# Kernel tuning notes

Measured on AMD Instinct MI355X. Metric: run time of the kernel, lower is better.

## Reference

```python
import jax, jax.numpy as jnp
import numpy as np

B, S, D_IN, D_OUT = 4, 2048, 1024, 1024


def setup_inputs() -> dict:
    key = jax.random.key(0)
    kx, kq, kk, kv = jax.random.split(key, 4)
    scale = 1.0 / np.sqrt(D_IN)
    return {
        "x": jax.random.normal(kx, (B, S, D_IN), dtype=jnp.float32),
        "W_q": jax.random.normal(kq, (D_IN, D_OUT), dtype=jnp.float32) * scale,
        "W_k": jax.random.normal(kk, (D_IN, D_OUT), dtype=jnp.float32) * scale,
        "W_v": jax.random.normal(kv, (D_IN, D_OUT), dtype=jnp.float32) * scale,
    }


def reference(x, W_q, W_k, W_v):
    # QKV projections (Linear without bias): [B,S,D_out]
    q = jnp.einsum("bsd,de->bse", x, W_q)
    k = jnp.einsum("bsd,de->bse", x, W_k)
    v = jnp.einsum("bsd,de->bse", x, W_v)

    # Raw scores [B,S,S], causal mask (strict upper triangle -> -inf),
    # then scale by sqrt(d_k) and softmax, matching the torch order of ops.
    scores = jnp.einsum("bqd,bkd->bqk", q, k)
    seq = scores.shape[-1]
    causal = jnp.triu(jnp.ones((seq, seq), dtype=bool), k=1)
    scores = jnp.where(causal[None, :, :], -jnp.inf, scores)
    attn = jax.nn.softmax(scores / jnp.sqrt(jnp.asarray(q.shape[-1], scores.dtype)), axis=-1)
    # dropout p=0.0 -> identity (eval semantics)
    return jnp.einsum("bqk,bkd->bqd", attn, v)
```

## Files before the change

### kernel.cpp

```cpp
#include <hip/hip_runtime.h>

typedef unsigned short u16;
typedef __bf16 bf16x8 __attribute__((ext_vector_type(8)));
typedef float f32x4 __attribute__((ext_vector_type(4)));

__device__ __forceinline__ u16 f2bf(float f) {
    union { float f; unsigned int u; } v; v.f = f;
    unsigned int u = v.u;
    return (u16)((u + 0x7FFFu + ((u >> 16) & 1u)) >> 16);
}

__device__ __forceinline__ void load_lds16(const void* g, void* l) {
    __builtin_amdgcn_global_load_lds(
        (const __attribute__((address_space(1))) unsigned int*)g,
        (__attribute__((address_space(3))) unsigned int*)l,
        16, 0, 0);
}

__constant__ unsigned char cls_m[24] = {15,15,7,14,14,13,13,6,12,12,11,11,5,10,10,9,9,4,8,8,3,2,1,0};
__constant__ unsigned char cls_h[24] = { 0, 1,2, 0, 1, 0, 1,2, 0, 1, 0, 1,2, 0, 1,0,1,2,0,1,2,2,2,2};

__global__ void __launch_bounds__(256) prep_kernel(
    const float4* __restrict__ X, u16* __restrict__ xb,
    const float* __restrict__ Wq, const float* __restrict__ Wk,
    const float* __restrict__ Wv,
    u16* __restrict__ Oq, u16* __restrict__ Ok, u16* __restrict__ Ov,
    float* __restrict__ rowsum) {
    __shared__ float tile[32][33];
    const int bid = blockIdx.x, tid = threadIdx.x;
    if (bid < 8192) {
        int idx = bid * 256 + tid;
        float4 v = X[idx];
        ushort4 o;
        o.x = f2bf(v.x); o.y = f2bf(v.y); o.z = f2bf(v.z); o.w = f2bf(v.w);
        *(ushort4*)(xb + (size_t)idx * 4) = o;
    } else if (bid < 11264) {
        int id = bid - 8192;
        int zz = id >> 10;
        const float* W = (zz == 0) ? Wq : (zz == 1) ? Wk : Wv;
        u16* O = (zz == 0) ? Oq : (zz == 1) ? Ok : Ov;
        int n0 = (id & 31) * 32, k0 = ((id >> 5) & 31) * 32;
        int tx = tid & 31, ty = tid >> 5;
        #pragma unroll
        for (int j = 0; j < 32; j += 8)
            tile[ty + j][tx] = W[(size_t)(k0 + ty + j) * 1024 + n0 + tx];
        __syncthreads();
        #pragma unroll
        for (int j = 0; j < 32; j += 8)
            O[(size_t)(n0 + ty + j) * 1024 + k0 + tx] = f2bf(tile[tx][ty + j]);
    } else {
        rowsum[(bid - 11264) * 256 + tid] = 0.f;
    }
}

__global__ void __launch_bounds__(256) combine_kernel(
    const float4* __restrict__ P1, const float* __restrict__ rowsum,
    float4* __restrict__ out) {
    int b = blockIdx.x;
    int z = b >> 10;
    int i = (b & 1023) * 256 + threadIdx.x;
    int r = i >> 8;
    float inv = 1.0f / rowsum[z * 2048 + 1024 + r];
    size_t oi = (size_t)z * (2048 * 1024 / 4) + (1024 * 1024 / 4) + i;
    float4 a = out[oi];
    float4 p = P1[(size_t)z * (1024 * 1024 / 4) + i];
    a.x = (a.x + p.x) * inv;
    a.y = (a.y + p.y) * inv;
    a.z = (a.z + p.z) * inv;
    a.w = (a.w + p.w) * inv;
    out[oi] = a;
}

template <int MODE>
__global__ void __launch_bounds__(512) gemm_nt(
    const u16* __restrict__ xb, const u16* __restrict__ WqT,
    const u16* __restrict__ WkT, const u16* __restrict__ WvT,
    u16* __restrict__ Q, u16* __restrict__ Kb,
    u16* __restrict__ Vt, u16* __restrict__ S,
    float* __restrict__ rowsum, float* __restrict__ out,
    float* __restrict__ P1) {

    int mtile, ntile, z, kbeg = 0, kiters, kh = 2;
    const u16 *A, *B;

    if (MODE == 0) {
        int L = blockIdx.x;
        int c = L & 7, t = (L >> 3) & 7, hi = L >> 6;
        int p = hi * 8 + c;
        z = p >> 6; mtile = p & 63; ntile = t;
        A = xb;
        B = (z == 0) ? WqT : (z == 1) ? WkT : WvT;
        kiters = 16;
    } else if (MODE == 1) {
        int id2 = blockIdx.x;
        z = id2 / 192;
        int r = id2 - z * 192;
        int c = r & 7, g = r >> 3;
        if (g <= c)            { mtile = c;     ntile = g; }
        else if (g < 2*c + 10) { mtile = c + 8; ntile = g - (c + 1); }
        else return;
        A = Q  + (size_t)z * (2048 * 1024);
        B = Kb + (size_t)z * (2048 * 1024);
        kiters = 16;
    } else {
        int L = blockIdx.x;
        ntile = L & 7;
        int j = L >> 3;
        z = j & 3;
        int ci = j >> 2;
        mtile = cls_m[ci];
        kh = cls_h[ci];
        kbeg = (kh != 2) ? kh * (mtile + 1) : 0;
        kiters = (kh != 2) ? (mtile + 1) : (mtile + 1) * 2;
        A = S  + (size_t)z * (2048 * 2048);
        B = Vt + (size_t)z * (1024 * 2048);
    }

    const int LDA = (MODE == 2) ? 2048 : 1024;

    __shared__ __align__(16) u16 As[128 * 64];
    __shared__ __align__(16) u16 Bs[128 * 64 + MODE * 256];

    const int tid = threadIdx.x;
    const int lane = tid & 63;
    const int wave = tid >> 6;
    const int wr = wave >> 2, wc = wave & 3;

    const int r0 = tid >> 2;
    const int kb = (((tid & 3) ^ ((r0 >> 1) & 3))) * 16;

    const char* gA = (const char*)(A + (size_t)(mtile * 128 + r0) * LDA) + kb + kbeg * 128;
    const char* gB = (const char*)(B + (size_t)(ntile * 128 + r0) * LDA) + kb + kbeg * 128;

    char* lA = (char*)As + tid * 16;
    char* lB = (char*)Bs + tid * 16;

    f32x4 acc[4][2] = {};

    const int quad = lane >> 4;
    const int l16 = lane & 15;
    const int ch = quad ^ ((l16 >> 1) & 3);
    const int aoff = (wr * 64 + l16) * 32 + ch * 8;
    const int boff = (wc * 32 + l16) * 32 + ch * 8;

    for (int kt = 0; kt < kiters; ++kt) {
        load_lds16(gA,      lA);
        load_lds16(gA + 64, lA + 8192);
        load_lds16(gB,      lB);
        load_lds16(gB + 64, lB + 8192);
        gA += 128; gB += 128;
        __syncthreads();

        #pragma unroll
        for (int h = 0; h < 2; ++h) {
            const u16* ap = As + h * 4096 + aoff;
            const u16* bp = Bs + h * 4096 + boff;
            bf16x8 af[4], bfv[2];
            #pragma unroll
            for (int r = 0; r < 4; ++r) af[r] = *(const bf16x8*)(ap + r * 512);
            #pragma unroll
            for (int c = 0; c < 2; ++c) bfv[c] = *(const bf16x8*)(bp + c * 512);
            #pragma unroll
            for (int r = 0; r < 4; ++r)
                #pragma unroll
                for (int c = 0; c < 2; ++c)
                    acc[r][c] = __builtin_amdgcn_mfma_f32_16x16x32_bf16(
                        af[r], bfv[c], acc[r][c], 0, 0, 0);
        }
        __syncthreads();
    }

    const int grow0 = mtile * 128 + wr * 64 + quad * 4;
    const int gcol0 = ntile * 128 + wc * 32 + l16;

    if (MODE == 0) {
        if (z < 2) {
            u16* C = z ? Kb : Q;
            #pragma unroll
            for (int r = 0; r < 4; ++r)
                #pragma unroll
                for (int c = 0; c < 2; ++c)
                    #pragma unroll
                    for (int i = 0; i < 4; ++i)
                        C[(size_t)(grow0 + r * 16 + i) * 1024 + gcol0 + c * 16] =
                            f2bf(acc[r][c][i]);
        } else {
            #pragma unroll
            for (int r = 0; r < 4; ++r) {
                int m0 = grow0 + r * 16;
                int b = m0 >> 11, s0 = m0 & 2047;
                #pragma unroll
                for (int c = 0; c < 2; ++c) {
                    int d = gcol0 + c * 16;
                    ushort4 o;
                    o.x = f2bf(acc[r][c][0]); o.y = f2bf(acc[r][c][1]);
                    o.z = f2bf(acc[r][c][2]); o.w = f2bf(acc[r][c][3]);
                    *(ushort4*)(Vt + (size_t)b * (1024 * 2048) + (size_t)d * 2048 + s0) = o;
                }
            }
        }
    } else if (MODE == 1) {
        u16* C = S + (size_t)z * (2048 * 2048);
        float* rs = rowsum + z * 2048;
        const bool diag = (ntile == mtile);
        float rsum[4][4];
        #pragma unroll
        for (int r = 0; r < 4; ++r)
            #pragma unroll
            for (int i = 0; i < 4; ++i) rsum[r][i] = 0.f;
        #pragma unroll
        for (int r = 0; r < 4; ++r)
            #pragma unroll
            for (int c = 0; c < 2; ++c)
                #pragma unroll
                for (int i = 0; i < 4; ++i) {
                    int grow = grow0 + r * 16 + i;
                    int gcol = gcol0 + c * 16;
                    float e = 0.f;
                    if (!diag || gcol <= grow)
                        e = __expf(acc[r][c][i] * 0.03125f - 12.0f);
                    C[(size_t)grow * 2048 + gcol] = f2bf(e);
                    rsum[r][i] += e;
                }
        #pragma unroll
        for (int r = 0; r < 4; ++r)
            #pragma unroll
            for (int i = 0; i < 4; ++i) {
                float s = rsum[r][i];
                s += __shfl_xor(s, 1, 64);
                s += __shfl_xor(s, 2, 64);
                s += __shfl_xor(s, 4, 64);
                s += __shfl_xor(s, 8, 64);
                if (l16 == 0)
                    unsafeAtomicAdd(&rs[grow0 + r * 16 + i], s);
            }
    } else {
        if (kh == 2) {
            const float* rs = rowsum + z * 2048;
            float* C = out + (size_t)z * (2048 * 1024);
            #pragma unroll
            for (int r = 0; r < 4; ++r)
                #pragma unroll
                for (int i = 0; i < 4; ++i) {
                    int grow = grow0 + r * 16 + i;
                    float inv = 1.0f / rs[grow];
                    #pragma unroll
                    for (int c = 0; c < 2; ++c)
                        C[(size_t)grow * 1024 + gcol0 + c * 16] = acc[r][c][i] * inv;
                }
        } else if (kh == 1) {
            float* C = out + (size_t)z * (2048 * 1024);
            #pragma unroll
            for (int r = 0; r < 4; ++r)
                #pragma unroll
                for (int i = 0; i < 4; ++i) {
                    int grow = grow0 + r * 16 + i;
                    #pragma unroll
                    for (int c = 0; c < 2; ++c)
                        C[(size_t)grow * 1024 + gcol0 + c * 16] = acc[r][c][i];
                }
        } else {
            float* Pp = P1 + (size_t)z * (1024 * 1024);
            #pragma unroll
            for (int r = 0; r < 4; ++r)
                #pragma unroll
                for (int i = 0; i < 4; ++i) {
                    int prow = grow0 + r * 16 + i - 1024;
                    #pragma unroll
                    for (int c = 0; c < 2; ++c)
                        Pp[(size_t)prow * 1024 + gcol0 + c * 16] = acc[r][c][i];
                }
        }
    }
}

extern "C" void kernel_launch(void* const* d_in, const int* in_sizes, int n_in,
                              void* d_out, int out_size, void* d_ws, size_t ws_size,
                              hipStream_t stream) {
    const float* x  = (const float*)d_in[0];
    const float* Wq = (const float*)d_in[1];
    const float* Wk = (const float*)d_in[2];
    const float* Wv = (const float*)d_in[3];
    float* out = (float*)d_out;
    char* ws = (char*)d_ws;
    const size_t Mi = 1u << 20;

    u16* xb  = (u16*)(ws);
    u16* WqT = (u16*)(ws + 16 * Mi);
    u16* WkT = (u16*)(ws + 18 * Mi);
    u16* WvT = (u16*)(ws + 20 * Mi);
    u16* Q   = (u16*)(ws + 22 * Mi);
    u16* Kb  = (u16*)(ws + 38 * Mi);
    u16* Vt  = (u16*)(ws + 54 * Mi);
    u16* S   = (u16*)(ws + 70 * Mi);
    float* rowsum = (float*)(ws + 102 * Mi);
    float* P1 = (float*)xb;

    prep_kernel<<<11296, 256, 0, stream>>>(
        (const float4*)x, xb, Wq, Wk, Wv, WqT, WkT, WvT, rowsum);

    gemm_nt<0><<<1536, 512, 0, stream>>>(xb, WqT, WkT, WvT, Q, Kb, Vt, S, rowsum, out, P1);

    gemm_nt<1><<<768, 512, 0, stream>>>(xb, WqT, WkT, WvT, Q, Kb, Vt, S, rowsum, out, P1);

    gemm_nt<2><<<768, 512, 0, stream>>>(xb, WqT, WkT, WvT, Q, Kb, Vt, S, rowsum, out, P1);

    combine_kernel<<<4096, 256, 0, stream>>>(
        (const float4*)P1, rowsum, (float4*)out);
}
```

Before: 227.7 us.

## Use 256x256 double-buffered pipelined GEMM for scores and PV stages

Splits the QKV projection into its own kernel and gives the QK^T and PV GEMMs a new 256x256-tile kernel. The new kernel double-buffers operands in a 128KB LDS region, prefetches the next k-slices in sub-stages between MFMA groups, and uses explicit waitcnt, barriers and setprio for scheduling. Larger tiles raise arithmetic intensity and the pipeline hides global load latency. In exchange, launch counts drop to 256 and 192 blocks, which may underfill the GPU, and causal tiles now have coarser granularity.

```diff
diff --git a/kernel.cpp b/kernel.cpp
--- a/kernel.cpp
+++ b/kernel.cpp
@@ -17,8 +17,8 @@
         16, 0, 0);
 }
 
-__constant__ unsigned char cls_m[24] = {15,15,7,14,14,13,13,6,12,12,11,11,5,10,10,9,9,4,8,8,3,2,1,0};
-__constant__ unsigned char cls_h[24] = { 0, 1,2, 0, 1, 0, 1,2, 0, 1, 0, 1,2, 0, 1,0,1,2,0,1,2,2,2,2};
+__constant__ unsigned char c2m[12] = {7,7,3,6,6,5,5,2,4,4,1,0};
+__constant__ unsigned char c2h[12] = {0,1,2,0,1,0,1,2,0,1,2,2};
 
 __global__ void __launch_bounds__(256) prep_kernel(
     const float4* __restrict__ X, u16* __restrict__ xb,
@@ -71,55 +71,20 @@
     out[oi] = a;
 }
 
-template <int MODE>
-__global__ void __launch_bounds__(512) gemm_nt(
+__global__ void __launch_bounds__(512) gemm_qkv(
     const u16* __restrict__ xb, const u16* __restrict__ WqT,
     const u16* __restrict__ WkT, const u16* __restrict__ WvT,
-    u16* __restrict__ Q, u16* __restrict__ Kb,
-    u16* __restrict__ Vt, u16* __restrict__ S,
-    float* __restrict__ rowsum, float* __restrict__ out,
-    float* __restrict__ P1) {
-
-    int mtile, ntile, z, kbeg = 0, kiters, kh = 2;
-    const u16 *A, *B;
-
-    if (MODE == 0) {
-        int L = blockIdx.x;
-        int c = L & 7, t = (L >> 3) & 7, hi = L >> 6;
-        int p = hi * 8 + c;
-        z = p >> 6; mtile = p & 63; ntile = t;
-        A = xb;
-        B = (z == 0) ? WqT : (z == 1) ? WkT : WvT;
-        kiters = 16;
-    } else if (MODE == 1) {
-        int id2 = blockIdx.x;
-        z = id2 / 192;
-        int r = id2 - z * 192;
-        int c = r & 7, g = r >> 3;
-        if (g <= c)            { mtile = c;     ntile = g; }
-        else if (g < 2*c + 10) { mtile = c + 8; ntile = g - (c + 1); }
-        else return;
-        A = Q  + (size_t)z * (2048 * 1024);
-        B = Kb + (size_t)z * (2048 * 1024);
-        kiters = 16;
-    } else {
-        int L = blockIdx.x;
-        ntile = L & 7;
-        int j = L >> 3;
-        z = j & 3;
-        int ci = j >> 2;
-        mtile = cls_m[ci];
-        kh = cls_h[ci];
-        kbeg = (kh != 2) ? kh * (mtile + 1) : 0;
-        kiters = (kh != 2) ? (mtile + 1) : (mtile + 1) * 2;
-        A = S  + (size_t)z * (2048 * 2048);
-        B = Vt + (size_t)z * (1024 * 2048);
-    }
-
-    const int LDA = (MODE == 2) ? 2048 : 1024;
+    u16* __restrict__ Q, u16* __restrict__ Kb, u16* __restrict__ Vt) {
+
+    int L = blockIdx.x;
+    int c = L & 7, t = (L >> 3) & 7, hi = L >> 6;
+    int p = hi * 8 + c;
+    int z = p >> 6, mtile = p & 63, ntile = t;
+    const u16* A = xb;
+    const u16* B = (z == 0) ? WqT : (z == 1) ? WkT : WvT;
 
     __shared__ __align__(16) u16 As[128 * 64];
-    __shared__ __align__(16) u16 Bs[128 * 64 + MODE * 256];
+    __shared__ __align__(16) u16 Bs[128 * 64];
 
     const int tid = threadIdx.x;
     const int lane = tid & 63;
@@ -129,8 +94,8 @@
     const int r0 = tid >> 2;
     const int kb = (((tid & 3) ^ ((r0 >> 1) & 3))) * 16;
 
-    const char* gA = (const char*)(A + (size_t)(mtile * 128 + r0) * LDA) + kb + kbeg * 128;
-    const char* gB = (const char*)(B + (size_t)(ntile * 128 + r0) * LDA) + kb + kbeg * 128;
+    const char* gA = (const char*)(A + (size_t)(mtile * 128 + r0) * 1024) + kb;
+    const char* gB = (const char*)(B + (size_t)(ntile * 128 + r0) * 1024) + kb;
 
     char* lA = (char*)As + tid * 16;
     char* lB = (char*)Bs + tid * 16;
@@ -143,7 +108,7 @@
     const int aoff = (wr * 64 + l16) * 32 + ch * 8;
     const int boff = (wc * 32 + l16) * 32 + ch * 8;
 
-    for (int kt = 0; kt < kiters; ++kt) {
+    for (int kt = 0; kt < 16; ++kt) {
         load_lds16(gA,      lA);
         load_lds16(gA + 64, lA + 8192);
         load_lds16(gB,      lB);
@@ -159,13 +124,13 @@
             #pragma unroll
             for (int r = 0; r < 4; ++r) af[r] = *(const bf16x8*)(ap + r * 512);
             #pragma unroll
-            for (int c = 0; c < 2; ++c) bfv[c] = *(const bf16x8*)(bp + c * 512);
+            for (int cc = 0; cc < 2; ++cc) bfv[cc] = *(const bf16x8*)(bp + cc * 512);
             #pragma unroll
             for (int r = 0; r < 4; ++r)
                 #pragma unroll
-                for (int c = 0; c < 2; ++c)
-                    acc[r][c] = __builtin_amdgcn_mfma_f32_16x16x32_bf16(
-                        af[r], bfv[c], acc[r][c], 0, 0, 0);
+                for (int cc = 0; cc < 2; ++cc)
+                    acc[r][cc] = __builtin_amdgcn_mfma_f32_16x16x32_bf16(
+                        af[r], bfv[cc], acc[r][cc], 0, 0, 0);
         }
         __syncthreads();
     }
@@ -173,102 +138,258 @@
     const int grow0 = mtile * 128 + wr * 64 + quad * 4;
     const int gcol0 = ntile * 128 + wc * 32 + l16;
 
-    if (MODE == 0) {
-        if (z < 2) {
-            u16* C = z ? Kb : Q;
-            #pragma unroll
-            for (int r = 0; r < 4; ++r)
-                #pragma unroll
-                for (int c = 0; c < 2; ++c)
-                    #pragma unroll
-                    for (int i = 0; i < 4; ++i)
-                        C[(size_t)(grow0 + r * 16 + i) * 1024 + gcol0 + c * 16] =
-                            f2bf(acc[r][c][i]);
-        } else {
-            #pragma unroll
-            for (int r = 0; r < 4; ++r) {
-                int m0 = grow0 + r * 16;
-                int b = m0 >> 11, s0 = m0 & 2047;
-                #pragma unroll
-                for (int c = 0; c < 2; ++c) {
-                    int d = gcol0 + c * 16;
-                    ushort4 o;
-                    o.x = f2bf(acc[r][c][0]); o.y = f2bf(acc[r][c][1]);
-                    o.z = f2bf(acc[r][c][2]); o.w = f2bf(acc[r][c][3]);
-                    *(ushort4*)(Vt + (size_t)b * (1024 * 2048) + (size_t)d * 2048 + s0) = o;
-                }
+    if (z < 2) {
+        u16* C = z ? Kb : Q;
+        #pragma unroll
+        for (int r = 0; r < 4; ++r)
+            #pragma unroll
+            for (int cc = 0; cc < 2; ++cc)
+                #pragma unroll
+                for (int i = 0; i < 4; ++i)
+                    C[(size_t)(grow0 + r * 16 + i) * 1024 + gcol0 + cc * 16] =
+                        f2bf(acc[r][cc][i]);
+    } else {
+        #pragma unroll
+        for (int r = 0; r < 4; ++r) {
+            int m0 = grow0 + r * 16;
+            int b = m0 >> 11, s0 = m0 & 2047;
+            #pragma unroll
+            for (int cc = 0; cc < 2; ++cc) {
+                int d = gcol0 + cc * 16;
+                ushort4 o;
+                o.x = f2bf(acc[r][cc][0]); o.y = f2bf(acc[r][cc][1]);
+                o.z = f2bf(acc[r][cc][2]); o.w = f2bf(acc[r][cc][3]);
+                *(ushort4*)(Vt + (size_t)b * (1024 * 2048) + (size_t)d * 2048 + s0) = o;
             }
         }
-    } else if (MODE == 1) {
+    }
+}
+
+template <int MODE>
+__global__ void __launch_bounds__(512) gemm8(
+    const u16* __restrict__ Q, const u16* __restrict__ Kb,
+    const u16* __restrict__ Vt, u16* __restrict__ S,
+    float* __restrict__ rowsum, float* __restrict__ out,
+    float* __restrict__ P1) {
+
+    int mtile, ntile, z, kbeg = 0, nt, kh = 2;
+    const u16 *A, *B;
+    int LDA;
+
+    if (MODE == 1) {
+        int L = blockIdx.x;
+        z = L >> 6;
+        int w = L & 63;
+        mtile = w >> 3; ntile = w & 7;
+        if (ntile > mtile) return;
+        A = Q  + (size_t)z * (2048 * 1024);
+        B = Kb + (size_t)z * (2048 * 1024);
+        nt = 16; LDA = 1024;
+    } else {
+        int L = blockIdx.x;
+        ntile = L & 3;
+        z = (L >> 2) & 3;
+        int ci = L >> 4;
+        mtile = c2m[ci]; kh = c2h[ci];
+        int half = 2 * (mtile + 1);
+        if (kh == 0)      { kbeg = 0;    nt = half; }
+        else if (kh == 1) { kbeg = half; nt = half; }
+        else              { kbeg = 0;    nt = 4 * (mtile + 1); }
+        A = S  + (size_t)z * (2048 * 2048);
+        B = Vt + (size_t)z * (1024 * 2048);
+        LDA = 2048;
+    }
+
+    __shared__ __align__(16) char LDSc[131072];
+
+    const int tid  = threadIdx.x;
+    const int lane = tid & 63;
+    const int wave = tid >> 6;
+    const int wr = wave >> 2;
+    const int wc = wave & 3;
+    const int quad = lane >> 4, l16 = lane & 15;
+    const int ch = quad ^ ((l16 >> 1) & 3);
+
+    const int sl = tid >> 2;
+    const int sc = ((tid & 3) ^ ((sl >> 1) & 3)) * 16;
+    const int gAr = mtile * 256 + (sl & 63) + ((sl >> 6) << 7);
+    const int gBr = ntile * 256 + (sl & 31) + ((sl >> 5) << 6);
+    const char* gp0 = (const char*)(A + (size_t)gAr * LDA) + sc + kbeg * 128;
+    const char* gp1 = (const char*)(A + (size_t)(gAr + 64) * LDA) + sc + kbeg * 128;
+    const char* gp2 = (const char*)(B + (size_t)gBr * LDA) + sc + kbeg * 128;
+    const char* gp3 = (const char*)(B + (size_t)(gBr + 32) * LDA) + sc + kbeg * 128;
+
+#define STG(kind, gp, t) do { \
+        char* lb_ = LDSc + (((t) & 1) << 16) + ((kind) << 14) + tid * 16; \
+        const char* g_ = (gp) + (size_t)(t) * 128; \
+        load_lds16(g_,      lb_); \
+        load_lds16(g_ + 64, lb_ + 8192); } while (0)
+
+    const int aBase = (wr * 64 + l16) * 64 + ch * 16;
+    const int bBase = 32768 + (wc * 32 + l16) * 64 + ch * 16;
+
+    f32x4 acc[8][4] = {};
+    bf16x8 af[4][2], b0[2][2], b1[2][2];
+
+    STG(0, gp0, 0); STG(2, gp2, 0); STG(1, gp1, 0); STG(3, gp3, 0);
+    if (nt > 1) { STG(0, gp0, 1); STG(3, gp3, 1); STG(1, gp1, 1); }
+    if (nt > 1) asm volatile("s_waitcnt vmcnt(6)" ::: "memory");
+    else        asm volatile("s_waitcnt vmcnt(0)" ::: "memory");
+    __builtin_amdgcn_s_barrier();
+    __builtin_amdgcn_sched_barrier(0);
+
+    for (int u = 0; u < nt; ++u) {
+        const int bo = (u & 1) << 16;
+        #pragma unroll
+        for (int a = 0; a < 4; ++a)
+            #pragma unroll
+            for (int k = 0; k < 2; ++k)
+                af[a][k] = *(const bf16x8*)(LDSc + bo + k * 8192 + a * 1024 + aBase);
+        #pragma unroll
+        for (int f = 0; f < 2; ++f)
+            #pragma unroll
+            for (int k = 0; k < 2; ++k)
+                b0[f][k] = *(const bf16x8*)(LDSc + bo + k * 8192 + f * 1024 + bBase);
+        if (u + 1 < nt) STG(2, gp2, u + 1);
+        __builtin_amdgcn_s_barrier();
+        __builtin_amdgcn_s_setprio(1);
+        #pragma unroll
+        for (int k = 0; k < 2; ++k)
+            #pragma unroll
+            for (int a = 0; a < 4; ++a)
+                #pragma unroll
+                for (int f = 0; f < 2; ++f)
+                    acc[a][f] = __builtin_amdgcn_mfma_f32_16x16x32_bf16(
+                        af[a][k], b0[f][k], acc[a][f], 0, 0, 0);
+        __builtin_amdgcn_s_setprio(0);
+        __builtin_amdgcn_s_barrier();
+        __builtin_amdgcn_sched_barrier(0);
+        #pragma unroll
+        for (int f = 0; f < 2; ++f)
+            #pragma unroll
+            for (int k = 0; k < 2; ++k)
+                b1[f][k] = *(const bf16x8*)(LDSc + bo + 16384 + k * 8192 + f * 1024 + bBase);
+        if (u + 2 < nt) STG(0, gp0, u + 2);
+        __builtin_amdgcn_s_barrier();
+        __builtin_amdgcn_s_setprio(1);
+        #pragma unroll
+        for (int k = 0; k < 2; ++k)
+            #pragma unroll
+            for (int a = 0; a < 4; ++a)
+                #pragma unroll
+                for (int f = 0; f < 2; ++f)
+                    acc[a][2 + f] = __builtin_amdgcn_mfma_f32_16x16x32_bf16(
+                        af[a][k], b1[f][k], acc[a][2 + f], 0, 0, 0);
+        __builtin_amdgcn_s_setprio(0);
+        __builtin_amdgcn_s_barrier();
+        __builtin_amdgcn_sched_barrier(0);
+        #pragma unroll
+        for (int a = 0; a < 4; ++a)
+            #pragma unroll
+            for (int k = 0; k < 2; ++k)
+                af[a][k] = *(const bf16x8*)(LDSc + bo + 16384 + k * 8192 + a * 1024 + aBase);
+        if (u + 2 < nt) STG(3, gp3, u + 2);
+        __builtin_amdgcn_s_barrier();
+        __builtin_amdgcn_s_setprio(1);
+        #pragma unroll
+        for (int k = 0; k < 2; ++k)
+            #pragma unroll
+            for (int a = 0; a < 4; ++a)
+                #pragma unroll
+                for (int f = 0; f < 2; ++f)
+                    acc[4 + a][2 + f] = __builtin_amdgcn_mfma_f32_16x16x32_bf16(
+                        af[a][k], b1[f][k], acc[4 + a][2 + f], 0, 0, 0);
+        __builtin_amdgcn_s_setprio(0);
+        __builtin_amdgcn_s_barrier();
+        __builtin_amdgcn_sched_barrier(0);
+        #pragma unroll
+        for (int f = 0; f < 2; ++f)
+            #pragma unroll
+            for (int k = 0; k < 2; ++k)
+                b0[f][k] = *(const bf16x8*)(LDSc + bo + k * 8192 + f * 1024 + bBase);
+        if (u + 2 < nt) STG(1, gp1, u + 2);
+        __builtin_amdgcn_s_barrier();
+        __builtin_amdgcn_s_setprio(1);
+        #pragma unroll
+        for (int k = 0; k < 2; ++k)
+            #pragma unroll
+            for (int a = 0; a < 4; ++a)
+                #pragma unroll
+                for (int f = 0; f < 2; ++f)
+                    acc[4 + a][f] = __builtin_amdgcn_mfma_f32_16x16x32_bf16(
+                        af[a][k], b0[f][k], acc[4 + a][f], 0, 0, 0);
+        __builtin_amdgcn_s_setprio(0);
+        if (u + 2 < nt)      asm volatile("s_waitcnt vmcnt(6)" ::: "memory");
+        else if (u + 1 < nt) asm volatile("s_waitcnt vmcnt(0)" ::: "memory");
+        __builtin_amdgcn_s_barrier();
+        __builtin_amdgcn_sched_barrier(0);
+    }
+#undef STG
+
+    const int rb = mtile * 256 + wr * 128 + quad * 4;
+    const int cb = ntile * 256 + wc * 64 + l16;
+
+    if (MODE == 1) {
         u16* C = S + (size_t)z * (2048 * 2048);
         float* rs = rowsum + z * 2048;
         const bool diag = (ntile == mtile);
-        float rsum[4][4];
-        #pragma unroll
-        for (int r = 0; r < 4; ++r)
-            #pragma unroll
-            for (int i = 0; i < 4; ++i) rsum[r][i] = 0.f;
-        #pragma unroll
-        for (int r = 0; r < 4; ++r)
-            #pragma unroll
-            for (int c = 0; c < 2; ++c)
-                #pragma unroll
-                for (int i = 0; i < 4; ++i) {
-                    int grow = grow0 + r * 16 + i;
-                    int gcol = gcol0 + c * 16;
+        #pragma unroll
+        for (int ar = 0; ar < 8; ++ar)
+            #pragma unroll
+            for (int i = 0; i < 4; ++i) {
+                int grow = rb + (ar >> 2) * 64 + (ar & 3) * 16 + i;
+                float rsum = 0.f;
+                #pragma unroll
+                for (int c = 0; c < 4; ++c) {
+                    int gcol = cb + c * 16;
                     float e = 0.f;
                     if (!diag || gcol <= grow)
-                        e = __expf(acc[r][c][i] * 0.03125f - 12.0f);
+                        e = __expf(acc[ar][c][i] * 0.03125f - 12.0f);
                     C[(size_t)grow * 2048 + gcol] = f2bf(e);
-                    rsum[r][i] += e;
+                    rsum += e;
                 }
-        #pragma unroll
-        for (int r = 0; r < 4; ++r)
-            #pragma unroll
-            for (int i = 0; i < 4; ++i) {
-                float s = rsum[r][i];
-                s += __shfl_xor(s, 1, 64);
-                s += __shfl_xor(s, 2, 64);
-                s += __shfl_xor(s, 4, 64);
-                s += __shfl_xor(s, 8, 64);
+                rsum += __shfl_xor(rsum, 1, 64);
+                rsum += __shfl_xor(rsum, 2, 64);
+                rsum += __shfl_xor(rsum, 4, 64);
+                rsum += __shfl_xor(rsum, 8, 64);
                 if (l16 == 0)
-                    unsafeAtomicAdd(&rs[grow0 + r * 16 + i], s);
+                    unsafeAtomicAdd(&rs[grow], rsum);
             }
     } else {
         if (kh == 2) {
             const float* rs = rowsum + z * 2048;
             float* C = out + (size_t)z * (2048 * 1024);
             #pragma unroll
-            for (int r = 0; r < 4; ++r)
+            for (int ar = 0; ar < 8; ++ar)
                 #pragma unroll
                 for (int i = 0; i < 4; ++i) {
-                    int grow = grow0 + r * 16 + i;
+                    int grow = rb + (ar >> 2) * 64 + (ar & 3) * 16 + i;
                     float inv = 1.0f / rs[grow];
                     #pragma unroll
-                    for (int c = 0; c < 2; ++c)
-                        C[(size_t)grow * 1024 + gcol0 + c * 16] = acc[r][c][i] * inv;
+                    for (int c = 0; c < 4; ++c)
+                        C[(size_t)grow * 1024 + cb + c * 16] = acc[ar][c][i] * inv;
                 }
         } else if (kh == 1) {
             float* C = out + (size_t)z * (2048 * 1024);
             #pragma unroll
-            for (int r = 0; r < 4; ++r)
+            for (int ar = 0; ar < 8; ++ar)
                 #pragma unroll
                 for (int i = 0; i < 4; ++i) {
-                    int grow = grow0 + r * 16 + i;
+                    int grow = rb + (ar >> 2) * 64 + (ar & 3) * 16 + i;
                     #pragma unroll
-                    for (int c = 0; c < 2; ++c)
-                        C[(size_t)grow * 1024 + gcol0 + c * 16] = acc[r][c][i];
+                    for (int c = 0; c < 4; ++c)
+                        C[(size_t)grow * 1024 + cb + c * 16] = acc[ar][c][i];
                 }
         } else {
             float* Pp = P1 + (size_t)z * (1024 * 1024);
             #pragma unroll
-            for (int r = 0; r < 4; ++r)
+            for (int ar = 0; ar < 8; ++ar)
                 #pragma unroll
                 for (int i = 0; i < 4; ++i) {
-                    int prow = grow0 + r * 16 + i - 1024;
+                    int prow = rb + (ar >> 2) * 64 + (ar & 3) * 16 + i - 1024;
                     #pragma unroll
-                    for (int c = 0; c < 2; ++c)
-                        Pp[(size_t)prow * 1024 + gcol0 + c * 16] = acc[r][c][i];
+                    for (int c = 0; c < 4; ++c)
+                        Pp[(size_t)prow * 1024 + cb + c * 16] = acc[ar][c][i];
                 }
         }
     }
@@ -299,11 +420,11 @@
     prep_kernel<<<11296, 256, 0, stream>>>(
         (const float4*)x, xb, Wq, Wk, Wv, WqT, WkT, WvT, rowsum);
 
-    gemm_nt<0><<<1536, 512, 0, stream>>>(xb, WqT, WkT, WvT, Q, Kb, Vt, S, rowsum, out, P1);
-
-    gemm_nt<1><<<768, 512, 0, stream>>>(xb, WqT, WkT, WvT, Q, Kb, Vt, S, rowsum, out, P1);
-
-    gemm_nt<2><<<768, 512, 0, stream>>>(xb, WqT, WkT, WvT, Q, Kb, Vt, S, rowsum, out, P1);
+    gemm_qkv<<<1536, 512, 0, stream>>>(xb, WqT, WkT, WvT, Q, Kb, Vt);
+
+    gemm8<1><<<256, 512, 0, stream>>>(Q, Kb, Vt, S, rowsum, out, P1);
+
+    gemm8<2><<<192, 512, 0, stream>>>(Q, Kb, Vt, S, rowsum, out, P1);
 
     combine_kernel<<<4096, 256, 0, stream>>>(
         (const float4*)P1, rowsum, (float4*)out);
```

Result: faster. 222.9 us (-2.1%).
